# Kernel tuning notes

Hardware: AMD Instinct MI355X
Metric: run time of the kernel (lower is better)

## Reference

```python
import jax, jax.numpy as jnp
import numpy as np

N = 50000
E = 500000
D = 128
L = 3
BN_EPS = 1e-5


def setup_inputs() -> dict:
    key = jax.random.key(0)
    ks = jax.random.split(key, 16)

    def xavier(k, shape):
        fan_in, fan_out = shape[-2], shape[-1]
        limit = float(np.sqrt(6.0 / (fan_in + fan_out)))
        return jax.random.uniform(k, shape, jnp.float32, -limit, limit)

    inp = {
        "x": jax.random.randint(ks[0], (N, 2), 0, 3),
        "edge_index": jax.random.randint(ks[1], (2, E), 0, N),
        "edge_attr": jax.random.randint(ks[2], (E, 2), 0, 3),
        # atom embeddings (xavier_uniform like torch init)
        "atom_emb0": xavier(ks[3], (120, D)),
        "atom_emb1": xavier(ks[4], (3, D)),
        # per-layer edge embeddings, stacked over layers
        "edge_emb0": xavier(ks[5], (L, 5, D)),
        "edge_emb1": xavier(ks[6], (L, 3, D)),
        # per-layer MLP: Linear(D, 2D) -> ReLU -> Linear(2D, D)
        "W1": xavier(ks[7], (L, D, 2 * D)),
        "b1": jnp.zeros((L, 2 * D), jnp.float32),
        "W2": xavier(ks[8], (L, 2 * D, D)),
        "b2": jnp.zeros((L, D), jnp.float32),
        # batchnorm affine params
        "gamma": jnp.ones((L, D), jnp.float32),
        "beta": jnp.zeros((L, D), jnp.float32),
    }
    return inp


def reference(x, edge_index, edge_attr, atom_emb0, atom_emb1,
              edge_emb0, edge_emb1, W1, b1, W2, b2, gamma, beta):
    n = x.shape[0]
    num_layer = W1.shape[0]

    # atom embedding: sum of per-attribute embeddings -> [N, D]
    h = atom_emb0[x[:, 0]] + atom_emb1[x[:, 1]]

    # add self loops: src/dst both get arange(N) appended
    loop = jnp.arange(n, dtype=edge_index.dtype)
    src = jnp.concatenate([edge_index[0], loop])  # [E+N]
    dst = jnp.concatenate([edge_index[1], loop])  # [E+N]
    # self-loop edge attr is [4, 0]
    ea0 = jnp.concatenate([edge_attr[:, 0], jnp.full((n,), 4, edge_attr.dtype)])
    ea1 = jnp.concatenate([edge_attr[:, 1], jnp.zeros((n,), edge_attr.dtype)])

    for l in range(num_layer):
        # edge embedding lookup + message = x_j + edge_attr, scatter-add to dst
        eemb = edge_emb0[l][ea0] + edge_emb1[l][ea1]          # [E+N, D]
        msg = h[src] + eemb                                   # gather + add
        aggr = jax.ops.segment_sum(msg, dst, num_segments=n)  # [N, D]
        # MLP update
        hid = jax.nn.relu(aggr @ W1[l] + b1[l])               # [N, 2D]
        out = hid @ W2[l] + b2[l]                             # [N, D]
        # BatchNorm1d (training mode: batch stats, biased variance)
        mean = jnp.mean(out, axis=0)
        var = jnp.mean(jnp.square(out - mean), axis=0)
        out = gamma[l] * (out - mean) * jax.lax.rsqrt(var + BN_EPS) + beta[l]
        # dropout with p=0 is identity; ReLU on all but last layer
        h = out if l == num_layer - 1 else jax.nn.relu(out)
    return h
```

## Files before the change

### kernel.cpp

```cpp
#include <hip/hip_runtime.h>

#define D 128
#define TWO_D 256
#define BN_EPS 1e-5f

typedef __attribute__((ext_vector_type(8))) short bf16x8;
typedef __attribute__((ext_vector_type(4))) float f32x4;

__device__ __forceinline__ float relu_f(float x) { return x > 0.f ? x : 0.f; }

__device__ __forceinline__ unsigned short f2bf(float f) {
    unsigned u = __builtin_bit_cast(unsigned, f);
    return (unsigned short)((u + 0x7FFFu + ((u >> 16) & 1u)) >> 16);
}
__device__ __forceinline__ float bf2f(unsigned s) {
    unsigned u = s << 16;
    return __builtin_bit_cast(float, u);
}
__device__ __forceinline__ unsigned pack2(float a, float b) {
    return (unsigned)f2bf(a) | ((unsigned)f2bf(b) << 16);
}

__global__ void atom_embed_kernel(const int* __restrict__ x,
                                  const float* __restrict__ emb0,
                                  const float* __restrict__ emb1,
                                  unsigned short* __restrict__ hbf, int n) {
    if (blockIdx.x == 0 && threadIdx.x < 64)
        reinterpret_cast<unsigned*>(hbf + (size_t)n * D)[threadIdx.x] = 0u;
    int idx = blockIdx.x * blockDim.x + threadIdx.x;
    if (idx >= n * 32) return;
    int node = idx >> 5;
    int d0 = (idx & 31) << 2;
    int i0 = x[node * 2 + 0];
    int i1 = x[node * 2 + 1];
    const float4 a = *reinterpret_cast<const float4*>(emb0 + (size_t)i0 * D + d0);
    const float4 b = *reinterpret_cast<const float4*>(emb1 + (size_t)i1 * D + d0);
    uint2 v;
    v.x = pack2(a.x + b.x, a.y + b.y);
    v.y = pack2(a.z + b.z, a.w + b.w);
    *reinterpret_cast<uint2*>(hbf + (size_t)node * D + d0) = v;
}

__global__ void hist_kernel(const int* __restrict__ ei, int* __restrict__ counts, int e_cnt) {
    int e = blockIdx.x * blockDim.x + threadIdx.x;
    if (e >= e_cnt) return;
    atomicAdd(counts + ei[e_cnt + e], 1);
}

__device__ __forceinline__ int pad8(int d) { return (d + 7) & ~7; }

__global__ __launch_bounds__(256) void bsum_kernel(const int* __restrict__ counts,
                                                   int* __restrict__ bsum, int n) {
    __shared__ int s[256];
    int t = threadIdx.x;
    int idx = blockIdx.x * 256 + t;
    s[t] = (idx < n) ? pad8(counts[idx]) : 0;
    __syncthreads();
    for (int off = 128; off > 0; off >>= 1) {
        if (t < off) s[t] += s[t + off];
        __syncthreads();
    }
    if (t == 0) bsum[blockIdx.x] = s[0];
}

__global__ __launch_bounds__(256) void bscan_kernel(const int* __restrict__ bsum,
                                                    int* __restrict__ bpre,
                                                    int* __restrict__ rpp, int nb, int n) {
    __shared__ int s[256];
    int t = threadIdx.x;
    s[t] = (t < nb) ? bsum[t] : 0;
    __syncthreads();
    for (int off = 1; off < 256; off <<= 1) {
        int v = (t >= off) ? s[t - off] : 0;
        __syncthreads();
        s[t] += v;
        __syncthreads();
    }
    bpre[t] = (t == 0) ? 0 : s[t - 1];
    if (t == 255) rpp[n] = s[255];
}

__global__ __launch_bounds__(256) void scan_apply_kernel(const int* __restrict__ counts,
                                                         const int* __restrict__ bpre,
                                                         int* __restrict__ rpp,
                                                         int* __restrict__ cursor, int n) {
    __shared__ int s[256];
    int t = threadIdx.x;
    int idx = blockIdx.x * 256 + t;
    int c = (idx < n) ? pad8(counts[idx]) : 0;
    s[t] = c;
    __syncthreads();
    for (int off = 1; off < 256; off <<= 1) {
        int v = (t >= off) ? s[t - off] : 0;
        __syncthreads();
        s[t] += v;
        __syncthreads();
    }
    if (idx < n) {
        int excl = bpre[blockIdx.x] + s[t] - c;
        rpp[idx] = excl;
        cursor[idx] = excl;
    }
}

__global__ void fill_kernel(const int* __restrict__ ei, const int* __restrict__ ea,
                            int* __restrict__ cursor,
                            unsigned short* __restrict__ ep,
                            unsigned char* __restrict__ eaidx, int e_cnt) {
    int e = blockIdx.x * blockDim.x + threadIdx.x;
    if (e >= e_cnt) return;
    int dst = ei[e_cnt + e];
    int src = ei[e];
    int aidx = ea[e * 2 + 0] * 3 + ea[e * 2 + 1];
    int pos = atomicAdd(cursor + dst, 1);
    ep[pos] = (unsigned short)src;
    eaidx[pos] = (unsigned char)aidx;
}

__global__ void pad_kernel(const int* __restrict__ cursor, const int* __restrict__ counts,
                           const int* __restrict__ rpp,
                           unsigned short* __restrict__ ep,
                           unsigned char* __restrict__ eaidx, int n) {
    int i = blockIdx.x * blockDim.x + threadIdx.x;
    if (i >= n) return;
    int b = cursor[i];
    int e = rpp[i] + pad8(counts[i]);
    unsigned short zr = (unsigned short)n;
    for (int j = b; j < e; ++j) { ep[j] = zr; eaidx[j] = 9; }
}

__global__ void cnts_build_kernel(const int* __restrict__ rpp,
                                  const int* __restrict__ counts,
                                  const unsigned char* __restrict__ eaidx,
                                  unsigned long long* __restrict__ cnts, int n) {
    int i = blockIdx.x * blockDim.x + threadIdx.x;
    if (i >= n) return;
    const int jb = rpp[i];
    const int nch = pad8(counts[i]) >> 3;
    unsigned long long c = 0ull;
    for (int ch = 0; ch < nch; ++ch) {
        unsigned long long v = *reinterpret_cast<const unsigned long long*>(eaidx + jb + 8 * ch);
        #pragma unroll
        for (int b = 0; b < 8; ++b) {
            int a = (int)((v >> (b * 8)) & 0xFFull);
            if (a < 8) c += 1ull << (a * 8);
        }
    }
    cnts[i] = c;
}

__global__ void frag_prep_kernel(const float* __restrict__ W1,
                                 const float* __restrict__ W2,
                                 unsigned short* __restrict__ w1f,
                                 unsigned short* __restrict__ w2f, int Lnum) {
    int tid = blockIdx.x * blockDim.x + threadIdx.x;
    if (tid >= Lnum * 128 * 64) return;
    int l = tid / 8192;
    int rem = tid % 8192;
    int frag = rem / 64;
    int lane = rem % 64;
    int kg = lane >> 4, cl = lane & 15;
    if (frag < 64) {
        int kk = frag >> 4, tn = frag & 15;
        const float* src = W1 + (size_t)l * D * TWO_D;
        int k0 = kk * 32 + kg * 8, col = tn * 16 + cl;
        unsigned short* dst = w1f + (size_t)l * 32768 + ((size_t)frag * 64 + lane) * 8;
        #pragma unroll
        for (int j = 0; j < 8; ++j) dst[j] = f2bf(src[(size_t)(k0 + j) * TWO_D + col]);
    } else {
        int f2 = frag - 64;
        int kk = f2 >> 3, tn = f2 & 7;
        const float* src = W2 + (size_t)l * TWO_D * D;
        int k0 = kk * 32 + kg * 8, col = tn * 16 + cl;
        unsigned short* dst = w2f + (size_t)l * 32768 + ((size_t)f2 * 64 + lane) * 8;
        #pragma unroll
        for (int j = 0; j < 8; ++j) dst[j] = f2bf(src[(size_t)(k0 + j) * D + col]);
    }
}

__global__ __launch_bounds__(256) void gather_kernel(
    const unsigned short* __restrict__ hbf,
    const float* __restrict__ ee0_l, const float* __restrict__ ee1_l,
    const int* __restrict__ rpp, const int* __restrict__ counts,
    const unsigned long long* __restrict__ cnts,
    const unsigned short* __restrict__ ep,
    unsigned short* __restrict__ aggrbf, float* __restrict__ stats, int n) {

    __shared__ float cee[16 * D];
    const int t = threadIdx.x;
    if (blockIdx.x == 0) stats[t] = 0.f;
    for (int i = t; i < 16 * D; i += 256) {
        int r = i >> 7, d = i & 127;
        cee[i] = (r < 15) ? ee0_l[(r / 3) * D + d] + ee1_l[(r % 3) * D + d]
                          : ee0_l[4 * D + d] + ee1_l[d];
    }
    __syncthreads();

    int node = blockIdx.x * 8 + (t >> 5);
    if (node >= n) return;
    int d0 = (t & 31) << 2;

    const int jb = rpp[node];
    const int deg = counts[node];
    const unsigned long long c0 = cnts[node];
    const int nch = pad8(deg) >> 3;

    float ax, ay, az, aw;
    {
        const float4 cs = *reinterpret_cast<const float4*>(cee + 15 * D + d0);
        uint2 hv = *reinterpret_cast<const uint2*>(hbf + (size_t)node * D + d0);
        ax = bf2f(hv.x & 0xffffu) + cs.x;
        ay = bf2f(hv.x >> 16)     + cs.y;
        az = bf2f(hv.y & 0xffffu) + cs.z;
        aw = bf2f(hv.y >> 16)     + cs.w;
    }

    int csum = 0;
    #pragma unroll
    for (int a = 0; a < 8; ++a) {
        int fc = (int)((c0 >> (a * 8)) & 0xFFull);
        csum += fc;
        float f = (float)fc;
        const float4 ev = *reinterpret_cast<const float4*>(cee + a * D + d0);
        ax += f * ev.x; ay += f * ev.y; az += f * ev.z; aw += f * ev.w;
    }
    {
        float f = (float)(deg - csum);
        const float4 ev = *reinterpret_cast<const float4*>(cee + 8 * D + d0);
        ax += f * ev.x; ay += f * ev.y; az += f * ev.z; aw += f * ev.w;
    }

#define ROWLD(s) (*reinterpret_cast<const uint2*>(hbf + (size_t)(s) * D + d0))
#define EACC(sv) do { \
        ax += bf2f((sv).x & 0xffffu); ay += bf2f((sv).x >> 16); \
        az += bf2f((sv).y & 0xffffu); aw += bf2f((sv).y >> 16); } while (0)
#define PROC(iv) do { \
        const uint2 s0 = ROWLD((iv).x & 0xFFFFu), s1 = ROWLD((iv).x >> 16); \
        const uint2 s2 = ROWLD((iv).y & 0xFFFFu), s3 = ROWLD((iv).y >> 16); \
        const uint2 s4 = ROWLD((iv).z & 0xFFFFu), s5 = ROWLD((iv).z >> 16); \
        const uint2 s6 = ROWLD((iv).w & 0xFFFFu), s7 = ROWLD((iv).w >> 16); \
        EACC(s0); EACC(s1); EACC(s2); EACC(s3); \
        EACC(s4); EACC(s5); EACC(s6); EACC(s7); } while (0)

    if (nch) {
        uint4 iv = *reinterpret_cast<const uint4*>(ep + jb);
        for (int c = 1; c < nch; ++c) {
            uint4 nx = *reinterpret_cast<const uint4*>(ep + jb + 8 * c);
            PROC(iv);
            iv = nx;
        }
        PROC(iv);
    }
#undef ROWLD
#undef EACC
#undef PROC

    uint2 o;
    o.x = pack2(ax, ay);
    o.y = pack2(az, aw);
    *reinterpret_cast<uint2*>(aggrbf + (size_t)node * D + d0) = o;
}

__global__ __launch_bounds__(256) void mlp_mfma_kernel(
    const unsigned short* __restrict__ aggrbf,
    const bf16x8* __restrict__ w1f, const bf16x8* __restrict__ w2f,
    const float* __restrict__ b1l, const float* __restrict__ b2l,
    float* __restrict__ outf, float* __restrict__ stats, int n) {

    __shared__ unsigned short hid[32 * TWO_D];
    __shared__ float sred[256];

    const int wave = threadIdx.x >> 6;
    const int lane = threadIdx.x & 63;
    const int arow = lane & 15;
    const int kgrp = lane >> 4;

    bf16x8 W1[4][4];
    #pragma unroll
    for (int kk = 0; kk < 4; ++kk)
        #pragma unroll
        for (int t = 0; t < 4; ++t)
            W1[kk][t] = w1f[(kk * 16 + wave * 4 + t) * 64 + lane];
    bf16x8 W2[8][2];
    #pragma unroll
    for (int kk = 0; kk < 8; ++kk)
        #pragma unroll
        for (int t = 0; t < 2; ++t)
            W2[kk][t] = w2f[(kk * 8 + wave * 2 + t) * 64 + lane];

    float b1v[4], b2v[2];
    #pragma unroll
    for (int t = 0; t < 4; ++t) b1v[t] = b1l[wave * 64 + t * 16 + arow];
    #pragma unroll
    for (int t = 0; t < 2; ++t) b2v[t] = b2l[wave * 32 + t * 16 + arow];

    float ps[2] = {0.f, 0.f}, pq[2] = {0.f, 0.f};

    const int tiles = n >> 4;
    const int npair = (tiles + 1) >> 1;
    for (int p = blockIdx.x; p < npair; p += gridDim.x) {
        const int t0i = 2 * p, t1i = 2 * p + 1;
        const bool has1 = (t1i < tiles);
        const size_t r0 = (size_t)t0i * 16, r1 = (size_t)t1i * 16;

        bf16x8 a0[4], a1[4];
        #pragma unroll
        for (int kk = 0; kk < 4; ++kk)
            a0[kk] = *reinterpret_cast<const bf16x8*>(
                aggrbf + (r0 + arow) * D + kk * 32 + kgrp * 8);
        if (has1) {
            #pragma unroll
            for (int kk = 0; kk < 4; ++kk)
                a1[kk] = *reinterpret_cast<const bf16x8*>(
                    aggrbf + (r1 + arow) * D + kk * 32 + kgrp * 8);
        }

        f32x4 acc1[4];
        #pragma unroll
        for (int t = 0; t < 4; ++t) acc1[t] = (f32x4){0.f, 0.f, 0.f, 0.f};
        #pragma unroll
        for (int kk = 0; kk < 4; ++kk)
            #pragma unroll
            for (int t = 0; t < 4; ++t)
                acc1[t] = __builtin_amdgcn_mfma_f32_16x16x32_bf16(a0[kk], W1[kk][t], acc1[t], 0, 0, 0);

        __syncthreads();
        #pragma unroll
        for (int t = 0; t < 4; ++t) {
            const int cc = wave * 64 + t * 16 + arow;
            #pragma unroll
            for (int r = 0; r < 4; ++r) {
                const int rr = kgrp * 4 + r;
                hid[(rr * TWO_D + cc) ^ ((rr & 7) << 3)] = f2bf(relu_f(acc1[t][r] + b1v[t]));
            }
        }
        if (has1) {
            #pragma unroll
            for (int t = 0; t < 4; ++t) acc1[t] = (f32x4){0.f, 0.f, 0.f, 0.f};
            #pragma unroll
            for (int kk = 0; kk < 4; ++kk)
                #pragma unroll
                for (int t = 0; t < 4; ++t)
                    acc1[t] = __builtin_amdgcn_mfma_f32_16x16x32_bf16(a1[kk], W1[kk][t], acc1[t], 0, 0, 0);
            #pragma unroll
            for (int t = 0; t < 4; ++t) {
                const int cc = wave * 64 + t * 16 + arow;
                #pragma unroll
                for (int r = 0; r < 4; ++r) {
                    const int rr = 16 + kgrp * 4 + r;
                    hid[(rr * TWO_D + cc) ^ ((rr & 7) << 3)] = f2bf(relu_f(acc1[t][r] + b1v[t]));
                }
            }
        }
        __syncthreads();

        {
            f32x4 acc2[2];
            #pragma unroll
            for (int t = 0; t < 2; ++t) acc2[t] = (f32x4){0.f, 0.f, 0.f, 0.f};
            #pragma unroll
            for (int kk = 0; kk < 8; ++kk) {
                bf16x8 a2 = *reinterpret_cast<const bf16x8*>(
                    hid + ((arow * TWO_D + kk * 32 + kgrp * 8) ^ ((arow & 7) << 3)));
                #pragma unroll
                for (int t = 0; t < 2; ++t)
                    acc2[t] = __builtin_amdgcn_mfma_f32_16x16x32_bf16(a2, W2[kk][t], acc2[t], 0, 0, 0);
            }
            #pragma unroll
            for (int t = 0; t < 2; ++t) {
                const int col = wave * 32 + t * 16 + arow;
                #pragma unroll
                for (int r = 0; r < 4; ++r) {
                    float v = acc2[t][r] + b2v[t];
                    outf[(r0 + kgrp * 4 + r) * D + col] = v;
                    ps[t] += v; pq[t] += v * v;
                }
            }
        }
        if (has1) {
            f32x4 acc2[2];
            #pragma unroll
            for (int t = 0; t < 2; ++t) acc2[t] = (f32x4){0.f, 0.f, 0.f, 0.f};
            #pragma unroll
            for (int kk = 0; kk < 8; ++kk) {
                bf16x8 a2 = *reinterpret_cast<const bf16x8*>(
                    hid + (((16 + arow) * TWO_D + kk * 32 + kgrp * 8) ^ ((arow & 7) << 3)));
                #pragma unroll
                for (int t = 0; t < 2; ++t)
                    acc2[t] = __builtin_amdgcn_mfma_f32_16x16x32_bf16(a2, W2[kk][t], acc2[t], 0, 0, 0);
            }
            #pragma unroll
            for (int t = 0; t < 2; ++t) {
                const int col = wave * 32 + t * 16 + arow;
                #pragma unroll
                for (int r = 0; r < 4; ++r) {
                    float v = acc2[t][r] + b2v[t];
                    outf[(r1 + kgrp * 4 + r) * D + col] = v;
                    ps[t] += v; pq[t] += v * v;
                }
            }
        }
    }

    sred[threadIdx.x] = 0.f;
    __syncthreads();
    #pragma unroll
    for (int t = 0; t < 2; ++t) {
        const int col = wave * 32 + t * 16 + arow;
        atomicAdd(sred + col, ps[t]);
        atomicAdd(sred + 128 + col, pq[t]);
    }
    __syncthreads();
    unsafeAtomicAdd(stats + threadIdx.x, sred[threadIdx.x]);
}

__global__ void bn_mid_kernel(const float* __restrict__ out,
                              const float* __restrict__ stats,
                              const float* __restrict__ gamma_l,
                              const float* __restrict__ beta_l,
                              float inv_n,
                              unsigned short* __restrict__ dsth, int n) {
    __shared__ float sbn[2 * D];
    int t = threadIdx.x;
    if (blockIdx.x == 0 && t >= 128 && t < 192)
        reinterpret_cast<unsigned*>(dsth + (size_t)n * D)[t - 128] = 0u;
    if (t < 128) {
        float mean = stats[t] * inv_n;
        float var  = stats[128 + t] * inv_n - mean * mean;
        float sc = gamma_l[t] * rsqrtf(var + BN_EPS);
        sbn[t] = sc;
        sbn[128 + t] = beta_l[t] - mean * sc;
    }
    __syncthreads();
    int idx = blockIdx.x * blockDim.x + t;
    if (idx >= n * 32) return;
    int d0 = (idx & 31) << 2;
    float4 v  = *reinterpret_cast<const float4*>(out + (size_t)idx * 4);
    float4 sc = *reinterpret_cast<const float4*>(sbn + d0);
    float4 sh = *reinterpret_cast<const float4*>(sbn + 128 + d0);
    uint2 o;
    o.x = pack2(relu_f(v.x * sc.x + sh.x), relu_f(v.y * sc.y + sh.y));
    o.y = pack2(relu_f(v.z * sc.z + sh.z), relu_f(v.w * sc.w + sh.w));
    *reinterpret_cast<uint2*>(dsth + (size_t)idx * 4) = o;
}

__global__ void bn_apply_final_kernel(const float* __restrict__ out,
                                      const float* __restrict__ stats,
                                      const float* __restrict__ gamma_l,
                                      const float* __restrict__ beta_l,
                                      float inv_n,
                                      float* __restrict__ dst, int n) {
    __shared__ float sbn[2 * D];
    int t = threadIdx.x;
    if (t < 128) {
        float mean = stats[t] * inv_n;
        float var  = stats[128 + t] * inv_n - mean * mean;
        float sc = gamma_l[t] * rsqrtf(var + BN_EPS);
        sbn[t] = sc;
        sbn[128 + t] = beta_l[t] - mean * sc;
    }
    __syncthreads();
    int idx = blockIdx.x * blockDim.x + t;
    if (idx >= n * 32) return;
    int d0 = (idx & 31) << 2;
    float4 v  = *reinterpret_cast<const float4*>(out + (size_t)idx * 4);
    float4 sc = *reinterpret_cast<const float4*>(sbn + d0);
    float4 sh = *reinterpret_cast<const float4*>(sbn + 128 + d0);
    *reinterpret_cast<float4*>(dst + (size_t)idx * 4) =
        make_float4(v.x * sc.x + sh.x, v.y * sc.y + sh.y,
                    v.z * sc.z + sh.z, v.w * sc.w + sh.w);
}

extern "C" void kernel_launch(void* const* d_in, const int* in_sizes, int n_in,
                              void* d_out, int out_size, void* d_ws, size_t ws_size,
                              hipStream_t stream) {
    const int*   x     = (const int*)d_in[0];
    const int*   ei    = (const int*)d_in[1];
    const int*   ea    = (const int*)d_in[2];
    const float* aemb0 = (const float*)d_in[3];
    const float* aemb1 = (const float*)d_in[4];
    const float* eemb0 = (const float*)d_in[5];
    const float* eemb1 = (const float*)d_in[6];
    const float* W1    = (const float*)d_in[7];
    const float* b1    = (const float*)d_in[8];
    const float* W2    = (const float*)d_in[9];
    const float* b2    = (const float*)d_in[10];
    const float* gamma = (const float*)d_in[11];
    const float* beta  = (const float*)d_in[12];

    const int n = in_sizes[0] / 2;
    const int e = in_sizes[1] / 2;
    const int L = in_sizes[8] / TWO_D;
    const float inv_n = 1.0f / (float)n;

    char* ws = (char*)d_ws;
    float* outb = (float*)ws;                      ws += (size_t)n * D * 4;
    unsigned short* buf0 = (unsigned short*)ws;    ws += (size_t)(n + 1) * D * 2;
    unsigned short* buf1 = (unsigned short*)ws;    ws += (size_t)(n + 1) * D * 2;
    unsigned short* bufC = (unsigned short*)ws;    ws += (size_t)n * D * 2;
    unsigned short* w1f = (unsigned short*)ws;     ws += (size_t)L * 32768 * 2;
    unsigned short* w2f = (unsigned short*)ws;     ws += (size_t)L * 32768 * 2;
    float* stats = (float*)ws;                     ws += 256 * 4;
    int* counts  = (int*)ws;                       ws += (size_t)n * 4;
    unsigned long long* cnts = (unsigned long long*)ws;  ws += (size_t)n * 8;
    int* rpp     = (int*)ws;                       ws += (size_t)(n + 4) * 4;
    int* cursor  = (int*)ws;                       ws += (size_t)n * 4;
    int* bsum    = (int*)ws;                       ws += 256 * 4;
    int* bpre    = (int*)ws;                       ws += 256 * 4;
    unsigned short* epack = (unsigned short*)ws;   ws += ((size_t)e + 8 * (size_t)n) * 2;
    unsigned char* eaidx  = (unsigned char*)ws;

    const int edge_blocks = (e + 255) / 256;
    const int vec_blocks  = (n * 32 + 255) / 256;
    const int node_blocks = (n + 7) / 8;
    const int nb = (n + 255) / 256;

    hipMemsetAsync(counts, 0, (size_t)n * 4, stream);
    hist_kernel<<<edge_blocks, 256, 0, stream>>>(ei, counts, e);
    bsum_kernel<<<nb, 256, 0, stream>>>(counts, bsum, n);
    bscan_kernel<<<1, 256, 0, stream>>>(bsum, bpre, rpp, nb, n);
    scan_apply_kernel<<<nb, 256, 0, stream>>>(counts, bpre, rpp, cursor, n);
    fill_kernel<<<edge_blocks, 256, 0, stream>>>(ei, ea, cursor, epack, eaidx, e);
    pad_kernel<<<nb, 256, 0, stream>>>(cursor, counts, rpp, epack, eaidx, n);
    cnts_build_kernel<<<nb, 256, 0, stream>>>(rpp, counts, eaidx, cnts, n);
    frag_prep_kernel<<<(L * 128 * 64 + 255) / 256, 256, 0, stream>>>(W1, W2, w1f, w2f, L);
    atom_embed_kernel<<<vec_blocks, 256, 0, stream>>>(x, aemb0, aemb1, buf0, n);

    for (int l = 0; l < L; ++l) {
        const float* ee0_l = eemb0 + (size_t)l * 5 * D;
        const float* ee1_l = eemb1 + (size_t)l * 3 * D;

        unsigned short* hsrc = (l & 1) ? buf1 : buf0;

        gather_kernel<<<node_blocks, 256, 0, stream>>>(
            hsrc, ee0_l, ee1_l, rpp, counts, cnts, epack, bufC, stats, n);
        mlp_mfma_kernel<<<512, 256, 0, stream>>>(
            bufC,
            (const bf16x8*)(w1f + (size_t)l * 32768),
            (const bf16x8*)(w2f + (size_t)l * 32768),
            b1 + (size_t)l * TWO_D, b2 + (size_t)l * D, outb, stats, n);

        if (l < L - 1) {
            unsigned short* hdst = (l & 1) ? buf0 : buf1;
            bn_mid_kernel<<<vec_blocks, 256, 0, stream>>>(
                outb, stats, gamma + (size_t)l * D, beta + (size_t)l * D,
                inv_n, hdst, n);
        } else {
            bn_apply_final_kernel<<<vec_blocks, 256, 0, stream>>>(
                outb, stats, gamma + (size_t)l * D, beta + (size_t)l * D,
                inv_n, (float*)d_out, n);
        }
    }
}
```

Baseline: 291.8 us.

## Fuse neighbor gather into MFMA MLP kernel via shared-memory aggregation tile

Merges the per-layer gather kernel and the MLP kernel into one persistent kernel. Each block gathers 32 node rows into a swizzled LDS tile and then runs both MFMA GEMMs on it, which removes the bf16 aggregation buffer round-trip through global memory and one launch per layer. Stats zeroing moves into atom_embed and bn_mid with ping-pong stats buffers. In exchange, weight fragments are reloaded from memory every tile instead of held for the whole kernel. The 512-block persistent grid also gives the latency-bound gather phase less parallelism, and gather and MMA phases in a block no longer overlap.

```diff
diff --git a/kernel.cpp b/kernel.cpp
--- a/kernel.cpp
+++ b/kernel.cpp
@@ -24,9 +24,13 @@
 __global__ void atom_embed_kernel(const int* __restrict__ x,
                                   const float* __restrict__ emb0,
                                   const float* __restrict__ emb1,
-                                  unsigned short* __restrict__ hbf, int n) {
-    if (blockIdx.x == 0 && threadIdx.x < 64)
-        reinterpret_cast<unsigned*>(hbf + (size_t)n * D)[threadIdx.x] = 0u;
+                                  unsigned short* __restrict__ hbf,
+                                  float* __restrict__ statsA, int n) {
+    if (blockIdx.x == 0) {
+        if (threadIdx.x < 64)
+            reinterpret_cast<unsigned*>(hbf + (size_t)n * D)[threadIdx.x] = 0u;
+        statsA[threadIdx.x] = 0.f;
+    }
     int idx = blockIdx.x * blockDim.x + threadIdx.x;
     if (idx >= n * 32) return;
     int node = idx >> 5;
@@ -178,59 +182,87 @@
     }
 }
 
-__global__ __launch_bounds__(256) void gather_kernel(
+__global__ __launch_bounds__(256) void fused_layer_kernel(
     const unsigned short* __restrict__ hbf,
     const float* __restrict__ ee0_l, const float* __restrict__ ee1_l,
     const int* __restrict__ rpp, const int* __restrict__ counts,
     const unsigned long long* __restrict__ cnts,
     const unsigned short* __restrict__ ep,
-    unsigned short* __restrict__ aggrbf, float* __restrict__ stats, int n) {
+    const bf16x8* __restrict__ w1f, const bf16x8* __restrict__ w2f,
+    const float* __restrict__ b1l, const float* __restrict__ b2l,
+    float* __restrict__ outf, float* __restrict__ stats, int n) {
 
     __shared__ float cee[16 * D];
+    __shared__ unsigned short agg[32 * D];
+    __shared__ unsigned short hid[32 * TWO_D];
+    __shared__ float sred[256];
+
     const int t = threadIdx.x;
-    if (blockIdx.x == 0) stats[t] = 0.f;
     for (int i = t; i < 16 * D; i += 256) {
         int r = i >> 7, d = i & 127;
         cee[i] = (r < 15) ? ee0_l[(r / 3) * D + d] + ee1_l[(r % 3) * D + d]
                           : ee0_l[4 * D + d] + ee1_l[d];
     }
-    __syncthreads();
-
-    int node = blockIdx.x * 8 + (t >> 5);
-    if (node >= n) return;
-    int d0 = (t & 31) << 2;
-
-    const int jb = rpp[node];
-    const int deg = counts[node];
-    const unsigned long long c0 = cnts[node];
-    const int nch = pad8(deg) >> 3;
-
-    float ax, ay, az, aw;
-    {
-        const float4 cs = *reinterpret_cast<const float4*>(cee + 15 * D + d0);
-        uint2 hv = *reinterpret_cast<const uint2*>(hbf + (size_t)node * D + d0);
-        ax = bf2f(hv.x & 0xffffu) + cs.x;
-        ay = bf2f(hv.x >> 16)     + cs.y;
-        az = bf2f(hv.y & 0xffffu) + cs.z;
-        aw = bf2f(hv.y >> 16)     + cs.w;
-    }
-
-    int csum = 0;
+
+    const int wave = t >> 6;
+    const int lane = t & 63;
+    const int arow = lane & 15;
+    const int kgrp = lane >> 4;
+    const int hw = t >> 5;
+    const int d0 = (t & 31) << 2;
+
+    float b1v[4], b2v[2];
     #pragma unroll
-    for (int a = 0; a < 8; ++a) {
-        int fc = (int)((c0 >> (a * 8)) & 0xFFull);
-        csum += fc;
-        float f = (float)fc;
-        const float4 ev = *reinterpret_cast<const float4*>(cee + a * D + d0);
-        ax += f * ev.x; ay += f * ev.y; az += f * ev.z; aw += f * ev.w;
-    }
-    {
-        float f = (float)(deg - csum);
-        const float4 ev = *reinterpret_cast<const float4*>(cee + 8 * D + d0);
-        ax += f * ev.x; ay += f * ev.y; az += f * ev.z; aw += f * ev.w;
-    }
-
-#define ROWLD(s) (*reinterpret_cast<const uint2*>(hbf + (size_t)(s) * D + d0))
+    for (int tt = 0; tt < 4; ++tt) b1v[tt] = b1l[wave * 64 + tt * 16 + arow];
+    #pragma unroll
+    for (int tt = 0; tt < 2; ++tt) b2v[tt] = b2l[wave * 32 + tt * 16 + arow];
+
+    __syncthreads();
+
+    float ps[2] = {0.f, 0.f}, pq[2] = {0.f, 0.f};
+
+    const int tiles = n >> 4;
+    const int npair = (tiles + 1) >> 1;
+
+    for (int p = blockIdx.x; p < npair; p += gridDim.x) {
+        const int row0 = p << 5;
+        const bool has1 = (row0 + 16 < n);
+
+        #pragma unroll 1
+        for (int s = 0; s < 4; ++s) {
+            const int nl = s * 8 + hw;
+            const int node = row0 + nl;
+            if (node < n) {
+                const int jb = rpp[node];
+                const int deg = counts[node];
+                const unsigned long long c0 = cnts[node];
+                const int nch = pad8(deg) >> 3;
+
+                float ax, ay, az, aw;
+                {
+                    const float4 cs = *reinterpret_cast<const float4*>(cee + 15 * D + d0);
+                    uint2 hv = *reinterpret_cast<const uint2*>(hbf + (size_t)node * D + d0);
+                    ax = bf2f(hv.x & 0xffffu) + cs.x;
+                    ay = bf2f(hv.x >> 16)     + cs.y;
+                    az = bf2f(hv.y & 0xffffu) + cs.z;
+                    aw = bf2f(hv.y >> 16)     + cs.w;
+                }
+                int csum = 0;
+                #pragma unroll
+                for (int a = 0; a < 8; ++a) {
+                    int fc = (int)((c0 >> (a * 8)) & 0xFFull);
+                    csum += fc;
+                    float f = (float)fc;
+                    const float4 ev = *reinterpret_cast<const float4*>(cee + a * D + d0);
+                    ax += f * ev.x; ay += f * ev.y; az += f * ev.z; aw += f * ev.w;
+                }
+                {
+                    float f = (float)(deg - csum);
+                    const float4 ev = *reinterpret_cast<const float4*>(cee + 8 * D + d0);
+                    ax += f * ev.x; ay += f * ev.y; az += f * ev.z; aw += f * ev.w;
+                }
+
+#define ROWLD(s_) (*reinterpret_cast<const uint2*>(hbf + (size_t)(s_) * D + d0))
 #define EACC(sv) do { \
         ax += bf2f((sv).x & 0xffffu); ay += bf2f((sv).x >> 16); \
         az += bf2f((sv).y & 0xffffu); aw += bf2f((sv).y >> 16); } while (0)
@@ -241,189 +273,165 @@
         const uint2 s6 = ROWLD((iv).w & 0xFFFFu), s7 = ROWLD((iv).w >> 16); \
         EACC(s0); EACC(s1); EACC(s2); EACC(s3); \
         EACC(s4); EACC(s5); EACC(s6); EACC(s7); } while (0)
-
-    if (nch) {
-        uint4 iv = *reinterpret_cast<const uint4*>(ep + jb);
-        for (int c = 1; c < nch; ++c) {
-            uint4 nx = *reinterpret_cast<const uint4*>(ep + jb + 8 * c);
-            PROC(iv);
-            iv = nx;
-        }
-        PROC(iv);
-    }
+                if (nch) {
+                    uint4 iv = *reinterpret_cast<const uint4*>(ep + jb);
+                    for (int c = 1; c < nch; ++c) {
+                        uint4 nx = *reinterpret_cast<const uint4*>(ep + jb + 8 * c);
+                        PROC(iv);
+                        iv = nx;
+                    }
+                    PROC(iv);
+                }
 #undef ROWLD
 #undef EACC
 #undef PROC
-
-    uint2 o;
-    o.x = pack2(ax, ay);
-    o.y = pack2(az, aw);
-    *reinterpret_cast<uint2*>(aggrbf + (size_t)node * D + d0) = o;
-}
-
-__global__ __launch_bounds__(256) void mlp_mfma_kernel(
-    const unsigned short* __restrict__ aggrbf,
-    const bf16x8* __restrict__ w1f, const bf16x8* __restrict__ w2f,
-    const float* __restrict__ b1l, const float* __restrict__ b2l,
-    float* __restrict__ outf, float* __restrict__ stats, int n) {
-
-    __shared__ unsigned short hid[32 * TWO_D];
-    __shared__ float sred[256];
-
-    const int wave = threadIdx.x >> 6;
-    const int lane = threadIdx.x & 63;
-    const int arow = lane & 15;
-    const int kgrp = lane >> 4;
-
-    bf16x8 W1[4][4];
-    #pragma unroll
-    for (int kk = 0; kk < 4; ++kk)
-        #pragma unroll
-        for (int t = 0; t < 4; ++t)
-            W1[kk][t] = w1f[(kk * 16 + wave * 4 + t) * 64 + lane];
-    bf16x8 W2[8][2];
-    #pragma unroll
-    for (int kk = 0; kk < 8; ++kk)
-        #pragma unroll
-        for (int t = 0; t < 2; ++t)
-            W2[kk][t] = w2f[(kk * 8 + wave * 2 + t) * 64 + lane];
-
-    float b1v[4], b2v[2];
-    #pragma unroll
-    for (int t = 0; t < 4; ++t) b1v[t] = b1l[wave * 64 + t * 16 + arow];
-    #pragma unroll
-    for (int t = 0; t < 2; ++t) b2v[t] = b2l[wave * 32 + t * 16 + arow];
-
-    float ps[2] = {0.f, 0.f}, pq[2] = {0.f, 0.f};
-
-    const int tiles = n >> 4;
-    const int npair = (tiles + 1) >> 1;
-    for (int p = blockIdx.x; p < npair; p += gridDim.x) {
-        const int t0i = 2 * p, t1i = 2 * p + 1;
-        const bool has1 = (t1i < tiles);
-        const size_t r0 = (size_t)t0i * 16, r1 = (size_t)t1i * 16;
+                uint2 o;
+                o.x = pack2(ax, ay);
+                o.y = pack2(az, aw);
+                *reinterpret_cast<uint2*>(agg + ((nl * D + d0) ^ ((nl & 7) << 3))) = o;
+            }
+        }
+
+        bf16x8 W1f[4][4];
+        #pragma unroll
+        for (int kk = 0; kk < 4; ++kk)
+            #pragma unroll
+            for (int tt = 0; tt < 4; ++tt)
+                W1f[kk][tt] = w1f[(kk * 16 + wave * 4 + tt) * 64 + lane];
+
+        __syncthreads();
 
         bf16x8 a0[4], a1[4];
         #pragma unroll
         for (int kk = 0; kk < 4; ++kk)
             a0[kk] = *reinterpret_cast<const bf16x8*>(
-                aggrbf + (r0 + arow) * D + kk * 32 + kgrp * 8);
+                agg + ((arow * D + kk * 32 + kgrp * 8) ^ ((arow & 7) << 3)));
         if (has1) {
             #pragma unroll
             for (int kk = 0; kk < 4; ++kk)
                 a1[kk] = *reinterpret_cast<const bf16x8*>(
-                    aggrbf + (r1 + arow) * D + kk * 32 + kgrp * 8);
+                    agg + (((16 + arow) * D + kk * 32 + kgrp * 8) ^ ((arow & 7) << 3)));
         }
 
         f32x4 acc1[4];
         #pragma unroll
-        for (int t = 0; t < 4; ++t) acc1[t] = (f32x4){0.f, 0.f, 0.f, 0.f};
+        for (int tt = 0; tt < 4; ++tt) acc1[tt] = (f32x4){0.f, 0.f, 0.f, 0.f};
         #pragma unroll
         for (int kk = 0; kk < 4; ++kk)
             #pragma unroll
-            for (int t = 0; t < 4; ++t)
-                acc1[t] = __builtin_amdgcn_mfma_f32_16x16x32_bf16(a0[kk], W1[kk][t], acc1[t], 0, 0, 0);
-
-        __syncthreads();
-        #pragma unroll
-        for (int t = 0; t < 4; ++t) {
-            const int cc = wave * 64 + t * 16 + arow;
+            for (int tt = 0; tt < 4; ++tt)
+                acc1[tt] = __builtin_amdgcn_mfma_f32_16x16x32_bf16(a0[kk], W1f[kk][tt], acc1[tt], 0, 0, 0);
+        #pragma unroll
+        for (int tt = 0; tt < 4; ++tt) {
+            const int cc = wave * 64 + tt * 16 + arow;
             #pragma unroll
             for (int r = 0; r < 4; ++r) {
                 const int rr = kgrp * 4 + r;
-                hid[(rr * TWO_D + cc) ^ ((rr & 7) << 3)] = f2bf(relu_f(acc1[t][r] + b1v[t]));
+                hid[(rr * TWO_D + cc) ^ ((rr & 7) << 3)] = f2bf(relu_f(acc1[tt][r] + b1v[tt]));
             }
         }
         if (has1) {
             #pragma unroll
-            for (int t = 0; t < 4; ++t) acc1[t] = (f32x4){0.f, 0.f, 0.f, 0.f};
+            for (int tt = 0; tt < 4; ++tt) acc1[tt] = (f32x4){0.f, 0.f, 0.f, 0.f};
             #pragma unroll
             for (int kk = 0; kk < 4; ++kk)
                 #pragma unroll
-                for (int t = 0; t < 4; ++t)
-                    acc1[t] = __builtin_amdgcn_mfma_f32_16x16x32_bf16(a1[kk], W1[kk][t], acc1[t], 0, 0, 0);
-            #pragma unroll
-            for (int t = 0; t < 4; ++t) {
-                const int cc = wave * 64 + t * 16 + arow;
+                for (int tt = 0; tt < 4; ++tt)
+                    acc1[tt] = __builtin_amdgcn_mfma_f32_16x16x32_bf16(a1[kk], W1f[kk][tt], acc1[tt], 0, 0, 0);
+            #pragma unroll
+            for (int tt = 0; tt < 4; ++tt) {
+                const int cc = wave * 64 + tt * 16 + arow;
                 #pragma unroll
                 for (int r = 0; r < 4; ++r) {
                     const int rr = 16 + kgrp * 4 + r;
-                    hid[(rr * TWO_D + cc) ^ ((rr & 7) << 3)] = f2bf(relu_f(acc1[t][r] + b1v[t]));
-                }
-            }
-        }
+                    hid[(rr * TWO_D + cc) ^ ((rr & 7) << 3)] = f2bf(relu_f(acc1[tt][r] + b1v[tt]));
+                }
+            }
+        }
+
+        bf16x8 W2f[8][2];
+        #pragma unroll
+        for (int kk = 0; kk < 8; ++kk)
+            #pragma unroll
+            for (int tt = 0; tt < 2; ++tt)
+                W2f[kk][tt] = w2f[(kk * 8 + wave * 2 + tt) * 64 + lane];
+
         __syncthreads();
 
         {
             f32x4 acc2[2];
             #pragma unroll
-            for (int t = 0; t < 2; ++t) acc2[t] = (f32x4){0.f, 0.f, 0.f, 0.f};
+            for (int tt = 0; tt < 2; ++tt) acc2[tt] = (f32x4){0.f, 0.f, 0.f, 0.f};
             #pragma unroll
             for (int kk = 0; kk < 8; ++kk) {
                 bf16x8 a2 = *reinterpret_cast<const bf16x8*>(
                     hid + ((arow * TWO_D + kk * 32 + kgrp * 8) ^ ((arow & 7) << 3)));
                 #pragma unroll
-                for (int t = 0; t < 2; ++t)
-                    acc2[t] = __builtin_amdgcn_mfma_f32_16x16x32_bf16(a2, W2[kk][t], acc2[t], 0, 0, 0);
-            }
-            #pragma unroll
-            for (int t = 0; t < 2; ++t) {
-                const int col = wave * 32 + t * 16 + arow;
+                for (int tt = 0; tt < 2; ++tt)
+                    acc2[tt] = __builtin_amdgcn_mfma_f32_16x16x32_bf16(a2, W2f[kk][tt], acc2[tt], 0, 0, 0);
+            }
+            #pragma unroll
+            for (int tt = 0; tt < 2; ++tt) {
+                const int col = wave * 32 + tt * 16 + arow;
                 #pragma unroll
                 for (int r = 0; r < 4; ++r) {
-                    float v = acc2[t][r] + b2v[t];
-                    outf[(r0 + kgrp * 4 + r) * D + col] = v;
-                    ps[t] += v; pq[t] += v * v;
+                    float v = acc2[tt][r] + b2v[tt];
+                    outf[((size_t)row0 + kgrp * 4 + r) * D + col] = v;
+                    ps[tt] += v; pq[tt] += v * v;
                 }
             }
         }
         if (has1) {
             f32x4 acc2[2];
             #pragma unroll
-            for (int t = 0; t < 2; ++t) acc2[t] = (f32x4){0.f, 0.f, 0.f, 0.f};
+            for (int tt = 0; tt < 2; ++tt) acc2[tt] = (f32x4){0.f, 0.f, 0.f, 0.f};
             #pragma unroll
             for (int kk = 0; kk < 8; ++kk) {
                 bf16x8 a2 = *reinterpret_cast<const bf16x8*>(
                     hid + (((16 + arow) * TWO_D + kk * 32 + kgrp * 8) ^ ((arow & 7) << 3)));
                 #pragma unroll
-                for (int t = 0; t < 2; ++t)
-                    acc2[t] = __builtin_amdgcn_mfma_f32_16x16x32_bf16(a2, W2[kk][t], acc2[t], 0, 0, 0);
-            }
-            #pragma unroll
-            for (int t = 0; t < 2; ++t) {
-                const int col = wave * 32 + t * 16 + arow;
+                for (int tt = 0; tt < 2; ++tt)
+                    acc2[tt] = __builtin_amdgcn_mfma_f32_16x16x32_bf16(a2, W2f[kk][tt], acc2[tt], 0, 0, 0);
+            }
+            #pragma unroll
+            for (int tt = 0; tt < 2; ++tt) {
+                const int col = wave * 32 + tt * 16 + arow;
                 #pragma unroll
                 for (int r = 0; r < 4; ++r) {
-                    float v = acc2[t][r] + b2v[t];
-                    outf[(r1 + kgrp * 4 + r) * D + col] = v;
-                    ps[t] += v; pq[t] += v * v;
-                }
-            }
-        }
-    }
-
-    sred[threadIdx.x] = 0.f;
+                    float v = acc2[tt][r] + b2v[tt];
+                    outf[((size_t)row0 + 16 + kgrp * 4 + r) * D + col] = v;
+                    ps[tt] += v; pq[tt] += v * v;
+                }
+            }
+        }
+    }
+
+    sred[t] = 0.f;
     __syncthreads();
     #pragma unroll
-    for (int t = 0; t < 2; ++t) {
-        const int col = wave * 32 + t * 16 + arow;
-        atomicAdd(sred + col, ps[t]);
-        atomicAdd(sred + 128 + col, pq[t]);
-    }
-    __syncthreads();
-    unsafeAtomicAdd(stats + threadIdx.x, sred[threadIdx.x]);
+    for (int tt = 0; tt < 2; ++tt) {
+        const int col = wave * 32 + tt * 16 + arow;
+        atomicAdd(sred + col, ps[tt]);
+        atomicAdd(sred + 128 + col, pq[tt]);
+    }
+    __syncthreads();
+    unsafeAtomicAdd(stats + t, sred[t]);
 }
 
 __global__ void bn_mid_kernel(const float* __restrict__ out,
                               const float* __restrict__ stats,
+                              float* __restrict__ stats_next,
                               const float* __restrict__ gamma_l,
                               const float* __restrict__ beta_l,
                               float inv_n,
                               unsigned short* __restrict__ dsth, int n) {
     __shared__ float sbn[2 * D];
     int t = threadIdx.x;
-    if (blockIdx.x == 0 && t >= 128 && t < 192)
-        reinterpret_cast<unsigned*>(dsth + (size_t)n * D)[t - 128] = 0u;
+    if (blockIdx.x == 0) {
+        stats_next[t] = 0.f;
+        if (t >= 128 && t < 192)
+            reinterpret_cast<unsigned*>(dsth + (size_t)n * D)[t - 128] = 0u;
+    }
     if (t < 128) {
         float mean = stats[t] * inv_n;
         float var  = stats[128 + t] * inv_n - mean * mean;
@@ -497,10 +505,10 @@
     float* outb = (float*)ws;                      ws += (size_t)n * D * 4;
     unsigned short* buf0 = (unsigned short*)ws;    ws += (size_t)(n + 1) * D * 2;
     unsigned short* buf1 = (unsigned short*)ws;    ws += (size_t)(n + 1) * D * 2;
-    unsigned short* bufC = (unsigned short*)ws;    ws += (size_t)n * D * 2;
     unsigned short* w1f = (unsigned short*)ws;     ws += (size_t)L * 32768 * 2;
     unsigned short* w2f = (unsigned short*)ws;     ws += (size_t)L * 32768 * 2;
-    float* stats = (float*)ws;                     ws += 256 * 4;
+    float* statsA = (float*)ws;                    ws += 256 * 4;
+    float* statsB = (float*)ws;                    ws += 256 * 4;
     int* counts  = (int*)ws;                       ws += (size_t)n * 4;
     unsigned long long* cnts = (unsigned long long*)ws;  ws += (size_t)n * 8;
     int* rpp     = (int*)ws;                       ws += (size_t)(n + 4) * 4;
@@ -512,7 +520,6 @@
 
     const int edge_blocks = (e + 255) / 256;
     const int vec_blocks  = (n * 32 + 255) / 256;
-    const int node_blocks = (n + 7) / 8;
     const int nb = (n + 255) / 256;
 
     hipMemsetAsync(counts, 0, (size_t)n * 4, stream);
@@ -524,30 +531,31 @@
     pad_kernel<<<nb, 256, 0, stream>>>(cursor, counts, rpp, epack, eaidx, n);
     cnts_build_kernel<<<nb, 256, 0, stream>>>(rpp, counts, eaidx, cnts, n);
     frag_prep_kernel<<<(L * 128 * 64 + 255) / 256, 256, 0, stream>>>(W1, W2, w1f, w2f, L);
-    atom_embed_kernel<<<vec_blocks, 256, 0, stream>>>(x, aemb0, aemb1, buf0, n);
+    atom_embed_kernel<<<vec_blocks, 256, 0, stream>>>(x, aemb0, aemb1, buf0, statsA, n);
 
     for (int l = 0; l < L; ++l) {
         const float* ee0_l = eemb0 + (size_t)l * 5 * D;
         const float* ee1_l = eemb1 + (size_t)l * 3 * D;
 
         unsigned short* hsrc = (l & 1) ? buf1 : buf0;
-
-        gather_kernel<<<node_blocks, 256, 0, stream>>>(
-            hsrc, ee0_l, ee1_l, rpp, counts, cnts, epack, bufC, stats, n);
-        mlp_mfma_kernel<<<512, 256, 0, stream>>>(
-            bufC,
+        float* stats_cur  = (l & 1) ? statsB : statsA;
+        float* stats_next = (l & 1) ? statsA : statsB;
+
+        fused_layer_kernel<<<512, 256, 0, stream>>>(
+            hsrc, ee0_l, ee1_l, rpp, counts, cnts, epack,
             (const bf16x8*)(w1f + (size_t)l * 32768),
             (const bf16x8*)(w2f + (size_t)l * 32768),
-            b1 + (size_t)l * TWO_D, b2 + (size_t)l * D, outb, stats, n);
+            b1 + (size_t)l * TWO_D, b2 + (size_t)l * D,
+            outb, stats_cur, n);
 
         if (l < L - 1) {
             unsigned short* hdst = (l & 1) ? buf0 : buf1;
             bn_mid_kernel<<<vec_blocks, 256, 0, stream>>>(
-                outb, stats, gamma + (size_t)l * D, beta + (size_t)l * D,
+                outb, stats_cur, stats_next, gamma + (size_t)l * D, beta + (size_t)l * D,
                 inv_n, hdst, n);
         } else {
             bn_apply_final_kernel<<<vec_blocks, 256, 0, stream>>>(
-                outb, stats, gamma + (size_t)l * D, beta + (size_t)l * D,
+                outb, stats_cur, gamma + (size_t)l * D, beta + (size_t)l * D,
                 inv_n, (float*)d_out, n);
         }
     }
```

Measured after the change: 376.8 us. +29.1%, slower.
